# Kernel tuning notes

Hardware: AMD Instinct MI355X
Metric: run time of the kernel (lower is better)

Reference implementation:

```python
import jax, jax.numpy as jnp
import numpy as np

T, B, I, H = 512, 64, 512, 512

def setup_inputs() -> dict:
    key = jax.random.key(0)
    k1, k2, k3 = jax.random.split(key, 3)
    # scale weights to keep tanh out of deep saturation
    return {
        "input": jax.random.normal(k1, (T, B, I), dtype=jnp.float32),
        "w_ih": jax.random.normal(k2, (H, I), dtype=jnp.float32) / np.sqrt(I),
        "w_hh": jax.random.normal(k3, (H, H), dtype=jnp.float32) / np.sqrt(H),
    }

def reference(input, w_ih, w_hh):
    # vanilla tanh RNN: h_t = tanh(x_t @ w_ih^T + h_{t-1} @ w_hh^T)
    batch = input.shape[1]
    h0 = jnp.zeros((batch, w_hh.shape[0]), dtype=input.dtype)

    def step(h_prev, x):
        h = jnp.tanh(x @ w_ih.T + h_prev @ w_hh.T)
        return h, h

    h_last, h_all = jax.lax.scan(step, h0, input)
    return h_all, h_last
```

## Files before the change

### kernel.cpp

```cpp
#include <hip/hip_runtime.h>
#include <cmath>

#define T_STEPS 512
#define BATCH   64
#define ISZ     512
#define HSZ     512
#define EXN     32768

__global__ __launch_bounds__(256) void rnn_xw_f32(const float* __restrict__ x,
                                                  const float* __restrict__ wih,
                                                  float* __restrict__ out) {
    __shared__ float As[32][68];
    __shared__ float Bs[32][68];

    const int tid = threadIdx.x;
    const int n0  = blockIdx.x * 64;
    const int m0  = blockIdx.y * 64;
    const int r0  = (tid & 15) * 4;
    const int c0  = (tid >> 4) * 4;
    const int sr  = tid >> 2;
    const int sc  = (tid & 3) * 8;

    float acc[4][4] = {};

    const float* ap = x   + (size_t)(m0 + sr) * ISZ + sc;
    const float* bp = wih + (size_t)(n0 + sr) * ISZ + sc;

    for (int k0 = 0; k0 < ISZ; k0 += 32) {
        const float4 a0 = *(const float4*)(ap + k0);
        const float4 a1 = *(const float4*)(ap + k0 + 4);
        const float4 b0 = *(const float4*)(bp + k0);
        const float4 b1 = *(const float4*)(bp + k0 + 4);
        __syncthreads();
        As[sc + 0][sr] = a0.x; As[sc + 1][sr] = a0.y;
        As[sc + 2][sr] = a0.z; As[sc + 3][sr] = a0.w;
        As[sc + 4][sr] = a1.x; As[sc + 5][sr] = a1.y;
        As[sc + 6][sr] = a1.z; As[sc + 7][sr] = a1.w;
        Bs[sc + 0][sr] = b0.x; Bs[sc + 1][sr] = b0.y;
        Bs[sc + 2][sr] = b0.z; Bs[sc + 3][sr] = b0.w;
        Bs[sc + 4][sr] = b1.x; Bs[sc + 5][sr] = b1.y;
        Bs[sc + 6][sr] = b1.z; Bs[sc + 7][sr] = b1.w;
        __syncthreads();

        #pragma unroll
        for (int k = 0; k < 32; ++k) {
            const float4 av = *(const float4*)&As[k][r0];
            const float4 bv = *(const float4*)&Bs[k][c0];
            const float a[4] = {av.x, av.y, av.z, av.w};
            const float b[4] = {bv.x, bv.y, bv.z, bv.w};
            #pragma unroll
            for (int i = 0; i < 4; ++i)
                #pragma unroll
                for (int j = 0; j < 4; ++j)
                    acc[i][j] = fmaf(a[i], b[j], acc[i][j]);
        }
    }

    #pragma unroll
    for (int i = 0; i < 4; ++i) {
        float4 v; v.x = acc[i][0]; v.y = acc[i][1]; v.z = acc[i][2]; v.w = acc[i][3];
        *(float4*)(out + (size_t)(m0 + r0 + i) * HSZ + n0 + c0) = v;
    }
}

__device__ __forceinline__ void ex_store(unsigned long long* w, float h, unsigned tag) {
    union { float f; unsigned u; } c; c.f = h;
    const unsigned long long v = ((unsigned long long)tag << 32) | (unsigned long long)c.u;
    __hip_atomic_store(w, v, __ATOMIC_RELAXED, __HIP_MEMORY_SCOPE_AGENT);
}

__global__ __launch_bounds__(512, 2) void rnn_rec(const float* __restrict__ whh,
                                                  float* __restrict__ out,
                                                  unsigned long long* __restrict__ ex) {
    __shared__ float hl[1024];
    __shared__ float red[1024];
    float4* hl4 = (float4*)hl;

    const int tid  = threadIdx.x;
    const int p    = blockIdx.x >> 3;
    const int g    = blockIdx.x & 7;
    const int j0   = g * 64;
    const int b    = tid & 1;
    const int jg   = (tid >> 1) & 15;
    const int kseg = tid >> 5;
    const int lane = tid & 63;
    const int wv   = tid >> 6;

    float4 w[4][8];
    #pragma unroll
    for (int jx = 0; jx < 4; ++jx) {
        const float* wr = whh + (size_t)(j0 + jg * 4 + jx) * HSZ + kseg * 32;
        #pragma unroll
        for (int i = 0; i < 8; ++i)
            w[jx][i] = *(const float4*)(wr + 4 * i);
    }

    const int fb = tid & 1;
    const int fj = (tid >> 1) & 63;

    unsigned long long* exw0 = ex + (size_t)(2 * p + 0) * 512 + tid;
    unsigned long long* exw1 = ex + (size_t)(2 * p + 1) * 512 + tid;

    for (int t = 0; t < T_STEPS; ++t) {
        float xwv = 0.f;
        if (tid < 128)
            xwv = out[((size_t)t * BATCH + 2 * p + fb) * HSZ + j0 + fj];

        float acc = 0.f;
        if (t > 0) {
            const size_t soff = (size_t)((t - 1) & 1) * EXN;
            unsigned long long v0 = __hip_atomic_load(exw0 + soff, __ATOMIC_RELAXED,
                                                      __HIP_MEMORY_SCOPE_AGENT);
            unsigned long long v1 = __hip_atomic_load(exw1 + soff, __ATOMIC_RELAXED,
                                                      __HIP_MEMORY_SCOPE_AGENT);
            while ((unsigned)(v0 >> 32) != (unsigned)t ||
                   (unsigned)(v1 >> 32) != (unsigned)t) {
                __builtin_amdgcn_s_sleep(1);
                v0 = __hip_atomic_load(exw0 + soff, __ATOMIC_RELAXED,
                                       __HIP_MEMORY_SCOPE_AGENT);
                v1 = __hip_atomic_load(exw1 + soff, __ATOMIC_RELAXED,
                                       __HIP_MEMORY_SCOPE_AGENT);
            }
            union { unsigned u; float f; } c0, c1;
            c0.u = (unsigned)v0; c1.u = (unsigned)v1;
            hl[tid]       = c0.f;
            hl[512 + tid] = c1.f;
            __syncthreads();

            float p4[4] = {0.f, 0.f, 0.f, 0.f};
            #pragma unroll
            for (int i = 0; i < 8; ++i) {
                const float4 h4 = hl4[b * 128 + kseg * 8 + i];
                #pragma unroll
                for (int jx = 0; jx < 4; ++jx) {
                    p4[jx] = fmaf(w[jx][i].x, h4.x, p4[jx]);
                    p4[jx] = fmaf(w[jx][i].y, h4.y, p4[jx]);
                    p4[jx] = fmaf(w[jx][i].z, h4.z, p4[jx]);
                    p4[jx] = fmaf(w[jx][i].w, h4.w, p4[jx]);
                }
            }
            #pragma unroll
            for (int jx = 0; jx < 4; ++jx)
                p4[jx] += __shfl_xor(p4[jx], 32, 64);
            if (lane < 32) {
                float4 v; v.x = p4[0]; v.y = p4[1]; v.z = p4[2]; v.w = p4[3];
                *(float4*)&red[(wv * 32 + lane) * 4] = v;
            }
            __syncthreads();
            if (tid < 128) {
                const int c = (fj >> 2) * 2 + fb;
                const int ji = fj & 3;
                #pragma unroll
                for (int w8 = 0; w8 < 8; ++w8)
                    acc += red[(w8 * 32 + c) * 4 + ji];
            }
        }

        if (tid < 128) {
            const float a2 = acc + xwv;
            const float e  = __expf(2.f * a2);
            const float hv = 1.f - 2.f / (e + 1.f);
            out[((size_t)t * BATCH + 2 * p + fb) * HSZ + j0 + fj] = hv;
            if (t < T_STEPS - 1)
                ex_store(ex + (size_t)(t & 1) * EXN + (size_t)(2 * p + fb) * 512 + j0 + fj,
                         hv, (unsigned)(t + 1));
            else
                out[(size_t)T_STEPS * BATCH * HSZ + (size_t)(2 * p + fb) * HSZ + j0 + fj] = hv;
        }
    }
}

extern "C" void kernel_launch(void* const* d_in, const int* in_sizes, int n_in,
                              void* d_out, int out_size, void* d_ws, size_t ws_size,
                              hipStream_t stream) {
    (void)in_sizes; (void)n_in; (void)out_size; (void)ws_size;
    const float* x    = (const float*)d_in[0];
    const float* wih  = (const float*)d_in[1];
    const float* whh  = (const float*)d_in[2];
    float*       out  = (float*)d_out;
    unsigned long long* ex = (unsigned long long*)d_ws;

    (void)hipMemsetAsync(d_ws, 0, 2 * EXN * sizeof(unsigned long long), stream);

    hipLaunchKernelGGL(rnn_xw_f32, dim3(8, 512), dim3(256), 0, stream, x, wih, out);
    hipLaunchKernelGGL(rnn_rec, dim3(256), dim3(512), 0, stream, whh, out, ex);
}
```

Before: 1.148 ms.

## Fuse input projection into persistent recurrent kernel and overlap it off critical path

Removes the separate x@W_ih GEMM kernel and instead has each persistent block hold both W_ih and W_hh slices in registers, computing the next step's input projection after publishing h_t so it overlaps the wait for other blocks. The per-step reduction is restructured into warp-shuffle folds over 16 k-segments with padded double-buffered shared memory, dropping one __syncthreads and the shared-memory reduction buffer. This avoids a global round trip of the projected inputs and a kernel launch. In exchange it doubles register pressure for the weights and puts extra FMA work inside the serial time loop.

After: 1.129 ms. No clear change (-1.7%).

```diff
diff --git a/kernel.cpp b/kernel.cpp
--- a/kernel.cpp
+++ b/kernel.cpp
@@ -7,106 +7,104 @@
 #define HSZ     512
 #define EXN     32768
 
-__global__ __launch_bounds__(256) void rnn_xw_f32(const float* __restrict__ x,
-                                                  const float* __restrict__ wih,
-                                                  float* __restrict__ out) {
-    __shared__ float As[32][68];
-    __shared__ float Bs[32][68];
-
-    const int tid = threadIdx.x;
-    const int n0  = blockIdx.x * 64;
-    const int m0  = blockIdx.y * 64;
-    const int r0  = (tid & 15) * 4;
-    const int c0  = (tid >> 4) * 4;
-    const int sr  = tid >> 2;
-    const int sc  = (tid & 3) * 8;
-
-    float acc[4][4] = {};
-
-    const float* ap = x   + (size_t)(m0 + sr) * ISZ + sc;
-    const float* bp = wih + (size_t)(n0 + sr) * ISZ + sc;
-
-    for (int k0 = 0; k0 < ISZ; k0 += 32) {
-        const float4 a0 = *(const float4*)(ap + k0);
-        const float4 a1 = *(const float4*)(ap + k0 + 4);
-        const float4 b0 = *(const float4*)(bp + k0);
-        const float4 b1 = *(const float4*)(bp + k0 + 4);
-        __syncthreads();
-        As[sc + 0][sr] = a0.x; As[sc + 1][sr] = a0.y;
-        As[sc + 2][sr] = a0.z; As[sc + 3][sr] = a0.w;
-        As[sc + 4][sr] = a1.x; As[sc + 5][sr] = a1.y;
-        As[sc + 6][sr] = a1.z; As[sc + 7][sr] = a1.w;
-        Bs[sc + 0][sr] = b0.x; Bs[sc + 1][sr] = b0.y;
-        Bs[sc + 2][sr] = b0.z; Bs[sc + 3][sr] = b0.w;
-        Bs[sc + 4][sr] = b1.x; Bs[sc + 5][sr] = b1.y;
-        Bs[sc + 6][sr] = b1.z; Bs[sc + 7][sr] = b1.w;
-        __syncthreads();
-
-        #pragma unroll
-        for (int k = 0; k < 32; ++k) {
-            const float4 av = *(const float4*)&As[k][r0];
-            const float4 bv = *(const float4*)&Bs[k][c0];
-            const float a[4] = {av.x, av.y, av.z, av.w};
-            const float b[4] = {bv.x, bv.y, bv.z, bv.w};
-            #pragma unroll
-            for (int i = 0; i < 4; ++i)
-                #pragma unroll
-                for (int j = 0; j < 4; ++j)
-                    acc[i][j] = fmaf(a[i], b[j], acc[i][j]);
-        }
-    }
-
-    #pragma unroll
-    for (int i = 0; i < 4; ++i) {
-        float4 v; v.x = acc[i][0]; v.y = acc[i][1]; v.z = acc[i][2]; v.w = acc[i][3];
-        *(float4*)(out + (size_t)(m0 + r0 + i) * HSZ + n0 + c0) = v;
-    }
-}
-
 __device__ __forceinline__ void ex_store(unsigned long long* w, float h, unsigned tag) {
     union { float f; unsigned u; } c; c.f = h;
     const unsigned long long v = ((unsigned long long)tag << 32) | (unsigned long long)c.u;
     __hip_atomic_store(w, v, __ATOMIC_RELAXED, __HIP_MEMORY_SCOPE_AGENT);
 }
 
-__global__ __launch_bounds__(512, 2) void rnn_rec(const float* __restrict__ whh,
-                                                  float* __restrict__ out,
-                                                  unsigned long long* __restrict__ ex) {
-    __shared__ float hl[1024];
-    __shared__ float red[1024];
-    float4* hl4 = (float4*)hl;
+__device__ __forceinline__ float dot_fold_pick(const float4 (&W)[2][8],
+                                               const float4* __restrict__ src,
+                                               int parbase4, int kseg,
+                                               int jxr, int br) {
+    float A00 = 0.f, A01 = 0.f, A10 = 0.f, A11 = 0.f;
+    const float4* s0 = src + parbase4 + kseg * 9;
+    const float4* s1 = s0 + 144;
+    #pragma unroll
+    for (int i = 0; i < 8; ++i) {
+        const float4 h0 = s0[i];
+        const float4 h1 = s1[i];
+        A00 = fmaf(W[0][i].x, h0.x, A00); A00 = fmaf(W[0][i].y, h0.y, A00);
+        A00 = fmaf(W[0][i].z, h0.z, A00); A00 = fmaf(W[0][i].w, h0.w, A00);
+        A01 = fmaf(W[0][i].x, h1.x, A01); A01 = fmaf(W[0][i].y, h1.y, A01);
+        A01 = fmaf(W[0][i].z, h1.z, A01); A01 = fmaf(W[0][i].w, h1.w, A01);
+        A10 = fmaf(W[1][i].x, h0.x, A10); A10 = fmaf(W[1][i].y, h0.y, A10);
+        A10 = fmaf(W[1][i].z, h0.z, A10); A10 = fmaf(W[1][i].w, h0.w, A10);
+        A11 = fmaf(W[1][i].x, h1.x, A11); A11 = fmaf(W[1][i].y, h1.y, A11);
+        A11 = fmaf(W[1][i].z, h1.z, A11); A11 = fmaf(W[1][i].w, h1.w, A11);
+    }
+    #pragma unroll
+    for (int d = 1; d < 16; d <<= 1) {
+        A00 += __shfl_xor(A00, d, 64);
+        A01 += __shfl_xor(A01, d, 64);
+        A10 += __shfl_xor(A10, d, 64);
+        A11 += __shfl_xor(A11, d, 64);
+    }
+    const float a0 = br ? A01 : A00;
+    const float a1 = br ? A11 : A10;
+    return jxr ? a1 : a0;
+}
+
+__global__ __launch_bounds__(512, 2) void rnn_fused(const float* __restrict__ x,
+                                                    const float* __restrict__ wih,
+                                                    const float* __restrict__ whh,
+                                                    float* __restrict__ out,
+                                                    unsigned long long* __restrict__ ex) {
+    __shared__ __align__(16) float hls[2304];
+    __shared__ __align__(16) float xss[2304];
+    const float4* hl4 = (const float4*)hls;
+    const float4* xs4 = (const float4*)xss;
 
     const int tid  = threadIdx.x;
     const int p    = blockIdx.x >> 3;
     const int g    = blockIdx.x & 7;
-    const int j0   = g * 64;
-    const int b    = tid & 1;
-    const int jg   = (tid >> 1) & 15;
-    const int kseg = tid >> 5;
-    const int lane = tid & 63;
-    const int wv   = tid >> 6;
+    const int kseg = tid & 15;
+    const int jg   = tid >> 4;
+    const int jb   = g * 64 + jg * 2;
 
-    float4 w[4][8];
+    float4 wh[2][8], wi[2][8];
     #pragma unroll
-    for (int jx = 0; jx < 4; ++jx) {
-        const float* wr = whh + (size_t)(j0 + jg * 4 + jx) * HSZ + kseg * 32;
+    for (int jx = 0; jx < 2; ++jx) {
+        const float* hr = whh + (size_t)(jb + jx) * HSZ + kseg * 32;
+        const float* ir = wih + (size_t)(jb + jx) * ISZ + kseg * 32;
         #pragma unroll
-        for (int i = 0; i < 8; ++i)
-            w[jx][i] = *(const float4*)(wr + 4 * i);
+        for (int i = 0; i < 8; ++i) {
+            wh[jx][i] = *(const float4*)(hr + 4 * i);
+            wi[jx][i] = *(const float4*)(ir + 4 * i);
+        }
     }
-
-    const int fb = tid & 1;
-    const int fj = (tid >> 1) & 63;
 
     unsigned long long* exw0 = ex + (size_t)(2 * p + 0) * 512 + tid;
     unsigned long long* exw1 = ex + (size_t)(2 * p + 1) * 512 + tid;
 
+    const int whf = ((tid >> 5) * 9 + ((tid >> 2) & 7)) * 4 + (tid & 3);
+
+    const int bx = tid >> 8;
+    const int io = (tid & 255) * 2;
+    const int xf = ((bx * 16 + (io >> 5)) * 9 + ((io >> 2) & 7)) * 4 + (io & 3);
+    const float* xsrc = x + (size_t)(2 * p + bx) * ISZ + io;
+
+    const int jxr  = kseg >> 1;
+    const int br   = kseg & 1;
+    const int outj = jb + (jxr & 1);
+    const int outb = 2 * p + br;
+    float* outp = out + (size_t)outb * HSZ + outj;
+    unsigned long long* exself = ex + (size_t)outb * 512 + outj;
+
+    {
+        const float2 v = *(const float2*)xsrc;
+        *(float2*)&xss[xf] = v;
+    }
+    __syncthreads();
+    float xwv = dot_fold_pick(wi, xs4, 0, kseg, jxr, br);
+
     for (int t = 0; t < T_STEPS; ++t) {
-        float xwv = 0.f;
-        if (tid < 128)
-            xwv = out[((size_t)t * BATCH + 2 * p + fb) * HSZ + j0 + fj];
+        const int  parh  = (t & 1) * 288;
+        const bool havex = (t < T_STEPS - 1);
 
-        float acc = 0.f;
+        float2 xv;
+        if (havex) xv = *(const float2*)(xsrc + (size_t)(t + 1) * (BATCH * ISZ));
+
         if (t > 0) {
             const size_t soff = (size_t)((t - 1) & 1) * EXN;
             unsigned long long v0 = __hip_atomic_load(exw0 + soff, __ATOMIC_RELAXED,
@@ -123,50 +121,29 @@
             }
             union { unsigned u; float f; } c0, c1;
             c0.u = (unsigned)v0; c1.u = (unsigned)v1;
-            hl[tid]       = c0.f;
-            hl[512 + tid] = c1.f;
-            __syncthreads();
+            hls[parh * 4 + whf]       = c0.f;
+            hls[parh * 4 + 576 + whf] = c1.f;
+        }
+        if (havex) *(float2*)&xss[((t + 1) & 1) * 1152 + xf] = xv;
+        __syncthreads();
 
-            float p4[4] = {0.f, 0.f, 0.f, 0.f};
-            #pragma unroll
-            for (int i = 0; i < 8; ++i) {
-                const float4 h4 = hl4[b * 128 + kseg * 8 + i];
-                #pragma unroll
-                for (int jx = 0; jx < 4; ++jx) {
-                    p4[jx] = fmaf(w[jx][i].x, h4.x, p4[jx]);
-                    p4[jx] = fmaf(w[jx][i].y, h4.y, p4[jx]);
-                    p4[jx] = fmaf(w[jx][i].z, h4.z, p4[jx]);
-                    p4[jx] = fmaf(w[jx][i].w, h4.w, p4[jx]);
-                }
-            }
-            #pragma unroll
-            for (int jx = 0; jx < 4; ++jx)
-                p4[jx] += __shfl_xor(p4[jx], 32, 64);
-            if (lane < 32) {
-                float4 v; v.x = p4[0]; v.y = p4[1]; v.z = p4[2]; v.w = p4[3];
-                *(float4*)&red[(wv * 32 + lane) * 4] = v;
-            }
-            __syncthreads();
-            if (tid < 128) {
-                const int c = (fj >> 2) * 2 + fb;
-                const int ji = fj & 3;
-                #pragma unroll
-                for (int w8 = 0; w8 < 8; ++w8)
-                    acc += red[(w8 * 32 + c) * 4 + ji];
-            }
-        }
+        float acc = 0.f;
+        if (t > 0)
+            acc = dot_fold_pick(wh, hl4, parh, kseg, jxr, br);
 
-        if (tid < 128) {
+        if (kseg < 4) {
             const float a2 = acc + xwv;
             const float e  = __expf(2.f * a2);
             const float hv = 1.f - 2.f / (e + 1.f);
-            out[((size_t)t * BATCH + 2 * p + fb) * HSZ + j0 + fj] = hv;
-            if (t < T_STEPS - 1)
-                ex_store(ex + (size_t)(t & 1) * EXN + (size_t)(2 * p + fb) * 512 + j0 + fj,
-                         hv, (unsigned)(t + 1));
+            outp[(size_t)t * (BATCH * HSZ)] = hv;
+            if (havex)
+                ex_store(exself + (size_t)(t & 1) * EXN, hv, (unsigned)(t + 1));
             else
-                out[(size_t)T_STEPS * BATCH * HSZ + (size_t)(2 * p + fb) * HSZ + j0 + fj] = hv;
+                out[(size_t)T_STEPS * BATCH * HSZ + (size_t)outb * HSZ + outj] = hv;
         }
+
+        if (havex)
+            xwv = dot_fold_pick(wi, xs4, ((t + 1) & 1) * 288, kseg, jxr, br);
     }
 }
 
@@ -174,14 +151,14 @@
                               void* d_out, int out_size, void* d_ws, size_t ws_size,
                               hipStream_t stream) {
     (void)in_sizes; (void)n_in; (void)out_size; (void)ws_size;
-    const float* x    = (const float*)d_in[0];
-    const float* wih  = (const float*)d_in[1];
-    const float* whh  = (const float*)d_in[2];
-    float*       out  = (float*)d_out;
+    const float* x   = (const float*)d_in[0];
+    const float* wih = (const float*)d_in[1];
+    const float* whh = (const float*)d_in[2];
+    float*       out = (float*)d_out;
     unsigned long long* ex = (unsigned long long*)d_ws;
 
     (void)hipMemsetAsync(d_ws, 0, 2 * EXN * sizeof(unsigned long long), stream);
 
-    hipLaunchKernelGGL(rnn_xw_f32, dim3(8, 512), dim3(256), 0, stream, x, wih, out);
-    hipLaunchKernelGGL(rnn_rec, dim3(256), dim3(512), 0, stream, whh, out, ex);
+    hipLaunchKernelGGL(rnn_fused, dim3(256), dim3(512), 0, stream,
+                       x, wih, whh, out, ex);
 }
```
